# Optimization experiments

Hardware: AMD Instinct MI355X
Metric: run time of the kernel (lower is better)

The kernel has to match this reference:

```python
import jax, jax.numpy as jnp
import numpy as np

N = 50000    # nodes
E = 640000   # edges (avg degree ~12.8)
D = 128      # feature dim (input = hidden = output)
L = 3        # num_layers
BN_EPS = 1e-5


def setup_inputs() -> dict:
    key = jax.random.key(0)
    ks = jax.random.split(key, 6)
    x = jax.random.normal(ks[0], (N, D), dtype=jnp.float32)
    edge_index = jax.random.randint(ks[1], (2, E), 0, N, dtype=jnp.int32)
    s = 1.0 / np.sqrt(D)
    # Weights stored as (in, out); equivalent to torch Linear's x @ W.T with W:(out,in).
    W1 = jax.random.normal(ks[2], (L, D, D), dtype=jnp.float32) * s
    b1 = jnp.zeros((L, D), dtype=jnp.float32)
    gamma = jnp.ones((L, D), dtype=jnp.float32)   # BatchNorm weight
    beta = jnp.zeros((L, D), dtype=jnp.float32)   # BatchNorm bias
    W2 = jax.random.normal(ks[3], (L, D, D), dtype=jnp.float32) * s
    b2 = jnp.zeros((L, D), dtype=jnp.float32)
    return {"x": x, "W1": W1, "b1": b1, "gamma": gamma, "beta": beta,
            "W2": W2, "b2": b2, "edge_index": edge_index}


def reference(x, W1, b1, gamma, beta, W2, b2, edge_index):
    src = edge_index[0]
    dst = edge_index[1]
    h = x
    for i in range(L):
        # GINConv aggregation: sum of source-node features into destinations, eps=0
        agg = jax.ops.segment_sum(h[src], dst, num_segments=N)   # [N, D]
        z = h + agg                                              # (1+eps)*x + sum_j x_j
        # MLP: Linear -> BatchNorm1d (training stats) -> ReLU -> Linear
        z = z @ W1[i] + b1[i]
        mu = jnp.mean(z, axis=0)
        var = jnp.mean((z - mu) ** 2, axis=0)                    # biased var (torch BN)
        z = (z - mu) * jax.lax.rsqrt(var + BN_EPS) * gamma[i] + beta[i]
        z = jax.nn.relu(z)
        z = z @ W2[i] + b2[i]
        # inter-layer ReLU (dropout_rate=0 -> identity)
        h = jax.nn.relu(z) if i < L - 1 else z
    return h
```

## Files before the change

### kernel.cpp

```cpp
#include <hip/hip_runtime.h>

#define D 128
#define BN_EPS 1e-5f
#define ELLW 64
#define SGRP 8

typedef __bf16 bf16_t;
typedef __bf16 bf16x8 __attribute__((ext_vector_type(8)));
typedef __bf16 bf16x4 __attribute__((ext_vector_type(4)));
typedef float floatx4 __attribute__((ext_vector_type(4)));

__global__ void prep(const float* __restrict__ x, bf16_t* __restrict__ hb,
                     const float* __restrict__ W1, const float* __restrict__ W2,
                     bf16_t* __restrict__ Wsw, int* __restrict__ deg,
                     float* __restrict__ stats, int N, int n4) {
  int i = blockIdx.x * blockDim.x + threadIdx.x;
  if (i < n4) {
    float4 v = ((const float4*)x)[i];
    bf16x4 p;
    p[0] = (bf16_t)v.x; p[1] = (bf16_t)v.y; p[2] = (bf16_t)v.z; p[3] = (bf16_t)v.w;
    *(bf16x4*)(hb + (size_t)4 * i) = p;
  }
  if (i < N) deg[i] = 0;
  if (i < 3 * SGRP * 256) stats[i] = 0.f;
  if (i < 6 * 16384) {
    int mat = i >> 14;
    int kn = i & 16383;
    int k = kn >> 7;
    int n = kn & 127;
    const float* Wm = (mat < 3) ? (W1 + (size_t)mat * 16384)
                                : (W2 + (size_t)(mat - 3) * 16384);
    float v = Wm[kn];
    int f = ((n >> 4) << 2) | (k >> 5);
    int ln = (((k >> 3) & 3) << 4) | (n & 15);
    int j = k & 7;
    Wsw[(size_t)mat * 16384 + ((f << 6) + ln) * 8 + j] = (bf16_t)v;
  }
}

__global__ void ell_fill(const int* __restrict__ src, const int* __restrict__ dst,
                         int* __restrict__ deg, int* __restrict__ ell, int E) {
  int e = blockIdx.x * blockDim.x + threadIdx.x;
  if (e < E) {
    int d = dst[e];
    int slot = atomicAdd(&deg[d], 1);
    if (slot < ELLW) ell[(size_t)d * ELLW + slot] = src[e];
  }
}

__global__ __launch_bounds__(256) void aggregate(
    const bf16_t* __restrict__ h, bf16_t* __restrict__ z,
    const int* __restrict__ ell, const int* __restrict__ deg, int Nn) {
  int node = blockIdx.x * 16 + (threadIdx.x >> 4);
  if (node >= Nn) return;
  int s = threadIdx.x & 15;
  int off = s << 3;
  int dg = deg[node]; if (dg > ELLW) dg = ELLW;
  const int* nb = ell + (size_t)node * ELLW;

  bf16x8 sv = *(const bf16x8*)(h + (size_t)node * D + off);
  float A[8], B[8];
#pragma unroll
  for (int j = 0; j < 8; ++j) { A[j] = (float)sv[j]; B[j] = 0.f; }

  int e = 0;
  for (; e + 8 <= dg; e += 8) {
    int4 ia = *(const int4*)(nb + e);
    int4 ib = *(const int4*)(nb + e + 4);
    bf16x8 v0 = *(const bf16x8*)(h + (size_t)ia.x * D + off);
    bf16x8 v1 = *(const bf16x8*)(h + (size_t)ia.y * D + off);
    bf16x8 v2 = *(const bf16x8*)(h + (size_t)ia.z * D + off);
    bf16x8 v3 = *(const bf16x8*)(h + (size_t)ia.w * D + off);
    bf16x8 v4 = *(const bf16x8*)(h + (size_t)ib.x * D + off);
    bf16x8 v5 = *(const bf16x8*)(h + (size_t)ib.y * D + off);
    bf16x8 v6 = *(const bf16x8*)(h + (size_t)ib.z * D + off);
    bf16x8 v7 = *(const bf16x8*)(h + (size_t)ib.w * D + off);
#pragma unroll
    for (int j = 0; j < 8; ++j) {
      A[j] += (float)v0[j]; B[j] += (float)v1[j];
      A[j] += (float)v2[j]; B[j] += (float)v3[j];
      A[j] += (float)v4[j]; B[j] += (float)v5[j];
      A[j] += (float)v6[j]; B[j] += (float)v7[j];
    }
  }
  for (; e + 4 <= dg; e += 4) {
    int4 i4 = *(const int4*)(nb + e);
    bf16x8 v0 = *(const bf16x8*)(h + (size_t)i4.x * D + off);
    bf16x8 v1 = *(const bf16x8*)(h + (size_t)i4.y * D + off);
    bf16x8 v2 = *(const bf16x8*)(h + (size_t)i4.z * D + off);
    bf16x8 v3 = *(const bf16x8*)(h + (size_t)i4.w * D + off);
#pragma unroll
    for (int j = 0; j < 8; ++j) {
      A[j] += (float)v0[j]; B[j] += (float)v1[j];
      A[j] += (float)v2[j]; B[j] += (float)v3[j];
    }
  }
  for (; e < dg; ++e) {
    bf16x8 v = *(const bf16x8*)(h + (size_t)nb[e] * D + off);
#pragma unroll
    for (int j = 0; j < 8; ++j) A[j] += (float)v[j];
  }

  bf16x8 o;
#pragma unroll
  for (int j = 0; j < 8; ++j) o[j] = (bf16_t)(A[j] + B[j]);
  *(bf16x8*)(z + (size_t)node * D + off) = o;
}

__global__ __launch_bounds__(256) void gemm1_stats(
    const bf16_t* __restrict__ Z, const bf16_t* __restrict__ Wsw1,
    const float* __restrict__ bias1, float* __restrict__ stats,
    int nStrips, int N) {
  __shared__ float sred[256];
  const int t = threadIdx.x;
  const int lane = t & 63;
  const int l15 = lane & 15;
  const int quad = lane >> 4;
  const int strip = blockIdx.x * 4 + (t >> 6);
  const bool active = strip < nStrips;

  sred[t] = 0.f;
  __syncthreads();

  bf16x8 a[4];
  const int row = strip * 16 + l15;
  if (active && row < N) {
#pragma unroll
    for (int kc = 0; kc < 4; ++kc)
      a[kc] = *(const bf16x8*)(Z + (size_t)row * D + kc * 32 + quad * 8);
  } else {
#pragma unroll
    for (int kc = 0; kc < 4; ++kc)
#pragma unroll
      for (int j = 0; j < 8; ++j) a[kc][j] = (bf16_t)0.f;
  }

  floatx4 acc[8];
#pragma unroll
  for (int nt = 0; nt < 8; ++nt) {
    float bv = bias1[nt * 16 + l15];
    acc[nt] = (floatx4){bv, bv, bv, bv};
  }
#pragma unroll
  for (int nt = 0; nt < 8; ++nt) {
#pragma unroll
    for (int kc = 0; kc < 4; ++kc) {
      bf16x8 b = *(const bf16x8*)(Wsw1 + (size_t)((nt * 4 + kc) * 64 + lane) * 8);
      acc[nt] = __builtin_amdgcn_mfma_f32_16x16x32_bf16(a[kc], b, acc[nt], 0, 0, 0);
    }
  }

  const int rowBase = strip * 16 + quad * 4;
#pragma unroll
  for (int nt = 0; nt < 8; ++nt) {
    int c = nt * 16 + l15;
    float s = 0.f, q = 0.f;
    if (active) {
#pragma unroll
      for (int r = 0; r < 4; ++r) {
        if (rowBase + r < N) {
          float v = acc[nt][r];
          s += v; q += v * v;
        }
      }
    }
    s += __shfl_xor(s, 16); s += __shfl_xor(s, 32);
    q += __shfl_xor(q, 16); q += __shfl_xor(q, 32);
    if (quad == 0) {
      atomicAdd(&sred[c], s);
      atomicAdd(&sred[128 + c], q);
    }
  }
  __syncthreads();
  atomicAdd(&stats[((blockIdx.x & (SGRP - 1)) << 8) + t], sred[t]);
}

__global__ __launch_bounds__(256) void mlp2r(
    const bf16_t* __restrict__ Z, const float* __restrict__ stats,
    const float* __restrict__ gamma, const float* __restrict__ beta,
    const bf16_t* __restrict__ Wsw1, const float* __restrict__ bias1,
    const bf16_t* __restrict__ Wsw2, const float* __restrict__ bias2,
    void* __restrict__ outp, int nStrips, int N, float invN,
    int relu_out, int fp32_out) {
  __shared__ bf16_t T[64][136];
  __shared__ float abL[256];
  const int t = threadIdx.x;
  const int wv = t >> 6;
  const int lane = t & 63;
  const int l15 = lane & 15;
  const int quad = lane >> 4;
  const int strip = blockIdx.x * 4 + wv;
  const bool active = strip < nStrips;

  if (t < 128) {
    float s0 = 0.f, q0 = 0.f;
#pragma unroll
    for (int g = 0; g < SGRP; ++g) {
      s0 += stats[(g << 8) + t];
      q0 += stats[(g << 8) + 128 + t];
    }
    float mu = s0 * invN;
    float var = fmaxf(q0 * invN - mu * mu, 0.f);
    float ai = gamma[t] * rsqrtf(var + BN_EPS);
    abL[t] = ai;
    abL[128 + t] = beta[t] - mu * ai;
  }

  bf16x8 a[4];
  const int row = strip * 16 + l15;
  if (active && row < N) {
#pragma unroll
    for (int kc = 0; kc < 4; ++kc)
      a[kc] = *(const bf16x8*)(Z + (size_t)row * D + kc * 32 + quad * 8);
  } else {
#pragma unroll
    for (int kc = 0; kc < 4; ++kc)
#pragma unroll
      for (int j = 0; j < 8; ++j) a[kc][j] = (bf16_t)0.f;
  }

  floatx4 acc[8];
#pragma unroll
  for (int nt = 0; nt < 8; ++nt) {
    float bv = bias1[nt * 16 + l15];
    acc[nt] = (floatx4){bv, bv, bv, bv};
  }
#pragma unroll
  for (int nt = 0; nt < 8; ++nt) {
#pragma unroll
    for (int kc = 0; kc < 4; ++kc) {
      bf16x8 b = *(const bf16x8*)(Wsw1 + (size_t)((nt * 4 + kc) * 64 + lane) * 8);
      acc[nt] = __builtin_amdgcn_mfma_f32_16x16x32_bf16(a[kc], b, acc[nt], 0, 0, 0);
    }
  }

  __syncthreads();

  float bnA[8], bnB[8];
#pragma unroll
  for (int nt = 0; nt < 8; ++nt) {
    int c = nt * 16 + l15;
    bnA[nt] = abL[c];
    bnB[nt] = abL[128 + c];
  }

  const int lr = wv * 16 + quad * 4;
#pragma unroll
  for (int nt = 0; nt < 8; ++nt) {
    int c = nt * 16 + l15;
#pragma unroll
    for (int r = 0; r < 4; ++r)
      T[lr + r][c] = (bf16_t)fmaxf(fmaf(acc[nt][r], bnA[nt], bnB[nt]), 0.f);
  }
  __syncthreads();

  bf16x8 a2[4];
#pragma unroll
  for (int kc = 0; kc < 4; ++kc)
    a2[kc] = *(const bf16x8*)&T[wv * 16 + l15][kc * 32 + quad * 8];

#pragma unroll
  for (int nt = 0; nt < 8; ++nt) {
    float bv = bias2[nt * 16 + l15];
    acc[nt] = (floatx4){bv, bv, bv, bv};
  }
#pragma unroll
  for (int nt = 0; nt < 8; ++nt) {
#pragma unroll
    for (int kc = 0; kc < 4; ++kc) {
      bf16x8 b = *(const bf16x8*)(Wsw2 + (size_t)((nt * 4 + kc) * 64 + lane) * 8);
      acc[nt] = __builtin_amdgcn_mfma_f32_16x16x32_bf16(a2[kc], b, acc[nt], 0, 0, 0);
    }
  }

  if (!active) return;
  const int rowBase = strip * 16 + quad * 4;
  if (fp32_out) {
    float* out = (float*)outp;
#pragma unroll
    for (int nt = 0; nt < 8; ++nt) {
      int c = nt * 16 + l15;
#pragma unroll
      for (int r = 0; r < 4; ++r) {
        int rw = rowBase + r;
        if (rw < N) {
          float v = acc[nt][r];
          if (relu_out) v = fmaxf(v, 0.f);
          out[(size_t)rw * D + c] = v;
        }
      }
    }
  } else {
    bf16_t* out = (bf16_t*)outp;
#pragma unroll
    for (int nt = 0; nt < 8; ++nt) {
      int c = nt * 16 + l15;
#pragma unroll
      for (int r = 0; r < 4; ++r) {
        int rw = rowBase + r;
        if (rw < N) {
          float v = acc[nt][r];
          if (relu_out) v = fmaxf(v, 0.f);
          out[(size_t)rw * D + c] = (bf16_t)v;
        }
      }
    }
  }
}

extern "C" void kernel_launch(void* const* d_in, const int* in_sizes, int n_in,
                              void* d_out, int out_size, void* d_ws, size_t ws_size,
                              hipStream_t stream) {
  const float* x     = (const float*)d_in[0];
  const float* W1    = (const float*)d_in[1];
  const float* b1    = (const float*)d_in[2];
  const float* gamma = (const float*)d_in[3];
  const float* beta  = (const float*)d_in[4];
  const float* W2    = (const float*)d_in[5];
  const float* b2    = (const float*)d_in[6];
  const int*   ei    = (const int*)d_in[7];

  const int N = in_sizes[0] / D;
  const int E = in_sizes[7] / 2;
  const int* src = ei;
  const int* dst = ei + E;

  char* ws = (char*)d_ws;
  size_t bufBytes = (size_t)N * D * sizeof(bf16_t);
  bf16_t* hb   = (bf16_t*)ws;
  bf16_t* zb   = (bf16_t*)(ws + bufBytes);
  int*    ell  = (int*)(ws + 2 * bufBytes);
  int*    deg  = (int*)((char*)ell + (size_t)N * ELLW * sizeof(int));
  float*  stats = (float*)((char*)deg + (size_t)N * sizeof(int));
  bf16_t* Wsw  = (bf16_t*)(stats + 3 * SGRP * 256);

  const int n4 = N * D / 4;
  const int prepBlocks = (n4 + 255) / 256;
  const int eb = (E + 255) / 256;
  const int aggBlocks = (N + 15) / 16;
  const int nStrips = (N + 15) / 16;
  const int gemmBlocks = (nStrips + 3) / 4;
  const float invN = 1.f / (float)N;

  prep<<<prepBlocks, 256, 0, stream>>>(x, hb, W1, W2, Wsw, deg, stats, N, n4);
  ell_fill<<<eb, 256, 0, stream>>>(src, dst, deg, ell, E);

  for (int i = 0; i < 3; ++i) {
    float* st = stats + (size_t)i * SGRP * 256;
    aggregate<<<aggBlocks, 256, 0, stream>>>(hb, zb, ell, deg, N);
    gemm1_stats<<<gemmBlocks, 256, 0, stream>>>(
        zb, Wsw + (size_t)i * 16384, b1 + (size_t)i * D, st, nStrips, N);
    void* Ob = (i == 2) ? d_out : (void*)hb;
    mlp2r<<<gemmBlocks, 256, 0, stream>>>(
        zb, st, gamma + (size_t)i * D, beta + (size_t)i * D,
        Wsw + (size_t)i * 16384, b1 + (size_t)i * D,
        Wsw + (size_t)(i + 3) * 16384, b2 + (size_t)i * D,
        Ob, nStrips, N, invN, (i < 2) ? 1 : 0, (i == 2) ? 1 : 0);
  }
}
```

Baseline: 297.9 us.

## Partition ELL neighbor lists into four source windows per node

Splits each node's ELL adjacency into four buckets keyed by which quarter of the node range the source falls in, with per-bucket degree counters. The aggregate kernel then walks the buckets in order, so gathers across concurrently running nodes tend to hit the same region of h, which should improve L2 locality. The cost is four degree loads per node, shorter inner loops with more remainder iterations, and a larger ELL buffer (128 ints per node instead of 64). It also risks silently dropping edges when more than 32 neighbors of one node land in the same window.

```diff
diff --git a/kernel.cpp b/kernel.cpp
--- a/kernel.cpp
+++ b/kernel.cpp
@@ -2,7 +2,8 @@
 
 #define D 128
 #define BN_EPS 1e-5f
-#define ELLW 64
+#define NW 4
+#define ELLW 32
 #define SGRP 8
 
 typedef __bf16 bf16_t;
@@ -12,7 +13,7 @@
 
 __global__ void prep(const float* __restrict__ x, bf16_t* __restrict__ hb,
                      const float* __restrict__ W1, const float* __restrict__ W2,
-                     bf16_t* __restrict__ Wsw, int* __restrict__ deg,
+                     bf16_t* __restrict__ Wsw, int* __restrict__ deg4,
                      float* __restrict__ stats, int N, int n4) {
   int i = blockIdx.x * blockDim.x + threadIdx.x;
   if (i < n4) {
@@ -21,7 +22,7 @@
     p[0] = (bf16_t)v.x; p[1] = (bf16_t)v.y; p[2] = (bf16_t)v.z; p[3] = (bf16_t)v.w;
     *(bf16x4*)(hb + (size_t)4 * i) = p;
   }
-  if (i < N) deg[i] = 0;
+  if (i < (N << 2)) deg4[i] = 0;
   if (i < 3 * SGRP * 256) stats[i] = 0.f;
   if (i < 6 * 16384) {
     int mat = i >> 14;
@@ -39,66 +40,72 @@
 }
 
 __global__ void ell_fill(const int* __restrict__ src, const int* __restrict__ dst,
-                         int* __restrict__ deg, int* __restrict__ ell, int E) {
+                         int* __restrict__ deg4, int* __restrict__ ell,
+                         int E, int winw) {
   int e = blockIdx.x * blockDim.x + threadIdx.x;
   if (e < E) {
     int d = dst[e];
-    int slot = atomicAdd(&deg[d], 1);
-    if (slot < ELLW) ell[(size_t)d * ELLW + slot] = src[e];
+    int s = src[e];
+    int w = s / winw;
+    int slot = atomicAdd(&deg4[(d << 2) + w], 1);
+    if (slot < ELLW) ell[((size_t)d << 7) + (w << 5) + slot] = s;
   }
 }
 
 __global__ __launch_bounds__(256) void aggregate(
     const bf16_t* __restrict__ h, bf16_t* __restrict__ z,
-    const int* __restrict__ ell, const int* __restrict__ deg, int Nn) {
+    const int* __restrict__ ell, const int* __restrict__ deg4, int Nn) {
   int node = blockIdx.x * 16 + (threadIdx.x >> 4);
   if (node >= Nn) return;
   int s = threadIdx.x & 15;
   int off = s << 3;
-  int dg = deg[node]; if (dg > ELLW) dg = ELLW;
-  const int* nb = ell + (size_t)node * ELLW;
+  const int* nbase = ell + ((size_t)node << 7);
 
   bf16x8 sv = *(const bf16x8*)(h + (size_t)node * D + off);
   float A[8], B[8];
 #pragma unroll
   for (int j = 0; j < 8; ++j) { A[j] = (float)sv[j]; B[j] = 0.f; }
 
-  int e = 0;
-  for (; e + 8 <= dg; e += 8) {
-    int4 ia = *(const int4*)(nb + e);
-    int4 ib = *(const int4*)(nb + e + 4);
-    bf16x8 v0 = *(const bf16x8*)(h + (size_t)ia.x * D + off);
-    bf16x8 v1 = *(const bf16x8*)(h + (size_t)ia.y * D + off);
-    bf16x8 v2 = *(const bf16x8*)(h + (size_t)ia.z * D + off);
-    bf16x8 v3 = *(const bf16x8*)(h + (size_t)ia.w * D + off);
-    bf16x8 v4 = *(const bf16x8*)(h + (size_t)ib.x * D + off);
-    bf16x8 v5 = *(const bf16x8*)(h + (size_t)ib.y * D + off);
-    bf16x8 v6 = *(const bf16x8*)(h + (size_t)ib.z * D + off);
-    bf16x8 v7 = *(const bf16x8*)(h + (size_t)ib.w * D + off);
-#pragma unroll
-    for (int j = 0; j < 8; ++j) {
-      A[j] += (float)v0[j]; B[j] += (float)v1[j];
-      A[j] += (float)v2[j]; B[j] += (float)v3[j];
-      A[j] += (float)v4[j]; B[j] += (float)v5[j];
-      A[j] += (float)v6[j]; B[j] += (float)v7[j];
-    }
-  }
-  for (; e + 4 <= dg; e += 4) {
-    int4 i4 = *(const int4*)(nb + e);
-    bf16x8 v0 = *(const bf16x8*)(h + (size_t)i4.x * D + off);
-    bf16x8 v1 = *(const bf16x8*)(h + (size_t)i4.y * D + off);
-    bf16x8 v2 = *(const bf16x8*)(h + (size_t)i4.z * D + off);
-    bf16x8 v3 = *(const bf16x8*)(h + (size_t)i4.w * D + off);
-#pragma unroll
-    for (int j = 0; j < 8; ++j) {
-      A[j] += (float)v0[j]; B[j] += (float)v1[j];
-      A[j] += (float)v2[j]; B[j] += (float)v3[j];
-    }
-  }
-  for (; e < dg; ++e) {
-    bf16x8 v = *(const bf16x8*)(h + (size_t)nb[e] * D + off);
-#pragma unroll
-    for (int j = 0; j < 8; ++j) A[j] += (float)v[j];
+  for (int w = 0; w < NW; ++w) {
+    int dg = deg4[(node << 2) + w]; if (dg > ELLW) dg = ELLW;
+    const int* nb = nbase + (w << 5);
+    int e = 0;
+    for (; e + 8 <= dg; e += 8) {
+      int4 ia = *(const int4*)(nb + e);
+      int4 ib = *(const int4*)(nb + e + 4);
+      bf16x8 v0 = *(const bf16x8*)(h + (size_t)ia.x * D + off);
+      bf16x8 v1 = *(const bf16x8*)(h + (size_t)ia.y * D + off);
+      bf16x8 v2 = *(const bf16x8*)(h + (size_t)ia.z * D + off);
+      bf16x8 v3 = *(const bf16x8*)(h + (size_t)ia.w * D + off);
+      bf16x8 v4 = *(const bf16x8*)(h + (size_t)ib.x * D + off);
+      bf16x8 v5 = *(const bf16x8*)(h + (size_t)ib.y * D + off);
+      bf16x8 v6 = *(const bf16x8*)(h + (size_t)ib.z * D + off);
+      bf16x8 v7 = *(const bf16x8*)(h + (size_t)ib.w * D + off);
+#pragma unroll
+      for (int j = 0; j < 8; ++j) {
+        A[j] += (float)v0[j]; B[j] += (float)v1[j];
+        A[j] += (float)v2[j]; B[j] += (float)v3[j];
+        A[j] += (float)v4[j]; B[j] += (float)v5[j];
+        A[j] += (float)v6[j]; B[j] += (float)v7[j];
+      }
+    }
+    for (; e + 4 <= dg; e += 4) {
+      int4 i4 = *(const int4*)(nb + e);
+      bf16x8 v0 = *(const bf16x8*)(h + (size_t)i4.x * D + off);
+      bf16x8 v1 = *(const bf16x8*)(h + (size_t)i4.y * D + off);
+      bf16x8 v2 = *(const bf16x8*)(h + (size_t)i4.z * D + off);
+      bf16x8 v3 = *(const bf16x8*)(h + (size_t)i4.w * D + off);
+#pragma unroll
+      for (int j = 0; j < 8; ++j) {
+        A[j] += (float)v0[j]; B[j] += (float)v1[j];
+        A[j] += (float)v2[j]; B[j] += (float)v3[j];
+      }
+    }
+    for (; e < dg; ++e) {
+      bf16x8 v = *(const bf16x8*)(h + (size_t)nb[e] * D + off);
+#pragma unroll
+      for (int j = 0; j < 8; ++j) A[j] += (float)v[j];
+    }
   }
 
   bf16x8 o;
@@ -330,8 +337,8 @@
   bf16_t* hb   = (bf16_t*)ws;
   bf16_t* zb   = (bf16_t*)(ws + bufBytes);
   int*    ell  = (int*)(ws + 2 * bufBytes);
-  int*    deg  = (int*)((char*)ell + (size_t)N * ELLW * sizeof(int));
-  float*  stats = (float*)((char*)deg + (size_t)N * sizeof(int));
+  int*    deg4 = (int*)((char*)ell + ((size_t)N << 7) * sizeof(int));
+  float*  stats = (float*)((char*)deg4 + ((size_t)N << 2) * sizeof(int));
   bf16_t* Wsw  = (bf16_t*)(stats + 3 * SGRP * 256);
 
   const int n4 = N * D / 4;
@@ -341,13 +348,14 @@
   const int nStrips = (N + 15) / 16;
   const int gemmBlocks = (nStrips + 3) / 4;
   const float invN = 1.f / (float)N;
-
-  prep<<<prepBlocks, 256, 0, stream>>>(x, hb, W1, W2, Wsw, deg, stats, N, n4);
-  ell_fill<<<eb, 256, 0, stream>>>(src, dst, deg, ell, E);
+  const int winw = (N + NW - 1) / NW;
+
+  prep<<<prepBlocks, 256, 0, stream>>>(x, hb, W1, W2, Wsw, deg4, stats, N, n4);
+  ell_fill<<<eb, 256, 0, stream>>>(src, dst, deg4, ell, E, winw);
 
   for (int i = 0; i < 3; ++i) {
     float* st = stats + (size_t)i * SGRP * 256;
-    aggregate<<<aggBlocks, 256, 0, stream>>>(hb, zb, ell, deg, N);
+    aggregate<<<aggBlocks, 256, 0, stream>>>(hb, zb, ell, deg4, N);
     gemm1_stats<<<gemmBlocks, 256, 0, stream>>>(
         zb, Wsw + (size_t)i * 16384, b1 + (size_t)i * D, st, nStrips, N);
     void* Ob = (i == 2) ? d_out : (void*)hb;
```

New measurement: 349.2 us. 17.2% more time.
